# Optimization experiments

Measured on AMD Instinct MI355X. Metric: run time of the kernel, lower is better.

## Reference

```python
import jax, jax.numpy as jnp
import numpy as np

N = 16384
IN_DIM = 64
OUT_DIM = 64
BN_EPS = 1e-5
LEAKY_SLOPE = 0.01


def setup_inputs() -> dict:
    key = jax.random.key(0)
    k_g, k_h, k_w, k_b = jax.random.split(key, 4)
    g = jax.random.uniform(k_g, (N, N), dtype=jnp.float32)  # dense nonneg adjacency
    h = jax.random.normal(k_h, (N, IN_DIM), dtype=jnp.float32)
    W = jax.random.normal(k_w, (OUT_DIM, IN_DIM), dtype=jnp.float32) * (1.0 / np.sqrt(IN_DIM))
    b = jax.random.normal(k_b, (OUT_DIM,), dtype=jnp.float32) * 0.01
    gamma = jnp.ones((IN_DIM,), dtype=jnp.float32)
    beta = jnp.zeros((IN_DIM,), dtype=jnp.float32)
    return {"g": g, "h": h, "W": W, "b": b, "gamma": gamma, "beta": beta}


def reference(g, h, W, b, gamma, beta):
    # BatchNorm1d in training mode: batch statistics over the node axis
    mean = h.mean(axis=0)
    var = jnp.mean(jnp.square(h - mean), axis=0)  # biased variance, as torch BN
    hn = (h - mean) * (gamma / jnp.sqrt(var + BN_EPS)) + beta

    # g <- g + I  (add self-loops on the diagonal, no dense eye materialized)
    idx = jnp.arange(g.shape[0])
    ga = g.at[idx, idx].add(1.0)

    # D^{-1/2} A D^{-1/2}: torch builds diag matrices and does two N^3 matmuls;
    # mathematically identical row/column scaling (same values, O(N^2)).
    d_inv_sqrt = jax.lax.rsqrt(ga.sum(axis=1))  # [N]
    gn = ga * d_inv_sqrt[:, None] * d_inv_sqrt[None, :]

    # Linear projection, propagate, LeakyReLU
    hp = hn @ W.T + b                     # [N, out_dim]
    out = gn @ hp                         # [N, out_dim]
    return jnp.where(out >= 0, out, LEAKY_SLOPE * out)
```

## Files before the change

### kernel.cpp

```cpp
#include <hip/hip_runtime.h>
#include <hip/hip_bf16.h>

#define GN 16384
#define GDIM 64

typedef __attribute__((ext_vector_type(8))) short bf16x8;
typedef __attribute__((ext_vector_type(4))) float f32x4;

typedef __attribute__((address_space(1))) const void GASV;
typedef __attribute__((address_space(3))) void LASV;

__device__ __forceinline__ unsigned short f2bf(float x) {
    unsigned int u = __builtin_bit_cast(unsigned int, x);
    u += 0x7fffu + ((u >> 16) & 1u);
    return (unsigned short)(u >> 16);
}

__device__ __forceinline__ short f2bf_hw(float x) {
    __hip_bfloat16 b = __float2bfloat16(x);
    return (short)__builtin_bit_cast(unsigned short, b);
}

__global__ void bn_partial(const float* __restrict__ h, float* __restrict__ ps,
                           float* __restrict__ pq) {
    int b = blockIdx.x, t = threadIdx.x;
    int col = t & 63, wr = t >> 6;
    float s = 0.f, q = 0.f;
    int base = b * 64;
    for (int rep = 0; rep < 16; ++rep) {
        int row = base + wr + rep * 4;
        float v = h[row * GDIM + col];
        s += v; q += v * v;
    }
    __shared__ float ls[4][64], lq[4][64];
    ls[wr][col] = s; lq[wr][col] = q;
    __syncthreads();
    if (t < 64) {
        ps[b * 64 + t] = ls[0][t] + ls[1][t] + ls[2][t] + ls[3][t];
        pq[b * 64 + t] = lq[0][t] + lq[1][t] + lq[2][t] + lq[3][t];
    }
}

__global__ void bn_finalize(const float* __restrict__ ps, const float* __restrict__ pq,
                            const float* __restrict__ W, const float* __restrict__ bvec,
                            const float* __restrict__ gamma, const float* __restrict__ beta,
                            float* __restrict__ Wp, float* __restrict__ bp) {
    int t = threadIdx.x;
    __shared__ float s_s[64], s_t2[64];
    if (t < 64) {
        float S = 0.f, Q = 0.f;
        for (int b = 0; b < 256; ++b) { S += ps[b * 64 + t]; Q += pq[b * 64 + t]; }
        float mean = S * (1.0f / 16384.0f);
        float var  = Q * (1.0f / 16384.0f) - mean * mean;
        float sc   = gamma[t] * rsqrtf(var + 1e-5f);
        s_s[t]  = sc;
        s_t2[t] = beta[t] - mean * sc;
    }
    __syncthreads();
    for (int k = 0; k < 16; ++k) {
        int idx = t + k * 256;
        Wp[idx] = s_s[idx & 63] * W[idx];
    }
    if (t < 64) {
        float acc = bvec[t];
        for (int c = 0; c < 64; ++c) acc += s_t2[c] * W[t * 64 + c];
        bp[t] = acc;
    }
}

__global__ void linear_hp(const float* __restrict__ h, const float* __restrict__ Wp,
                          const float* __restrict__ bpr, float* __restrict__ hp) {
    __shared__ float lw[64][65];
    __shared__ float lh[16][65];
    int t = threadIdx.x;
    int rb = blockIdx.x * 16;
    for (int k = 0; k < 16; ++k) {
        int idx = t + k * 256;
        lw[idx >> 6][idx & 63] = Wp[idx];
    }
    for (int k = 0; k < 4; ++k) {
        int idx = t + k * 256;
        lh[idx >> 6][idx & 63] = h[rb * GDIM + idx];
    }
    __syncthreads();
    int o = t & 63, rg = t >> 6;
    float a0 = 0.f, a1 = 0.f, a2 = 0.f, a3 = 0.f;
    for (int c = 0; c < 64; ++c) {
        float wv = lw[o][c];
        a0 += lh[rg][c]      * wv;
        a1 += lh[rg + 4][c]  * wv;
        a2 += lh[rg + 8][c]  * wv;
        a3 += lh[rg + 12][c] * wv;
    }
    float bb = bpr[o];
    hp[(rb + rg) * GDIM + o]      = a0 + bb;
    hp[(rb + rg + 4) * GDIM + o]  = a1 + bb;
    hp[(rb + rg + 8) * GDIM + o]  = a2 + bb;
    hp[(rb + rg + 12) * GDIM + o] = a3 + bb;
}

__global__ void rowsum_dinv(const float* __restrict__ g, float* __restrict__ dinv) {
    int row = blockIdx.x, t = threadIdx.x;
    const f32x4* grow = (const f32x4*)(g + (size_t)row * GN);
    float s = 0.f;
    for (int k = 0; k < 16; ++k) {
        f32x4 v = grow[t + k * 256];
        s += (v[0] + v[1]) + (v[2] + v[3]);
    }
    for (int off = 32; off; off >>= 1) s += __shfl_down(s, off, 64);
    __shared__ float wsum[4];
    if ((t & 63) == 0) wsum[t >> 6] = s;
    __syncthreads();
    if (t == 0) {
        float tot = (wsum[0] + wsum[1]) + (wsum[2] + wsum[3]) + 1.0f;
        dinv[row] = rsqrtf(tot);
    }
}

__global__ void make_hsT(const float* __restrict__ hp, const float* __restrict__ dinv,
                         unsigned short* __restrict__ hsT) {
    __shared__ float tile[64][65];
    int t = threadIdx.x;
    int jb = blockIdx.x * 64;
    int o = t & 63, jg = t >> 6;
    for (int k = 0; k < 16; ++k) {
        int j = jg + k * 4;
        tile[j][o] = hp[(jb + j) * GDIM + o] * dinv[jb + j];
    }
    __syncthreads();
    int oo = t >> 2, q = t & 3;
    for (int k = 0; k < 16; ++k) {
        int j = q * 16 + k;
        hsT[(size_t)oo * GN + jb + j] = f2bf(tile[j][oo]);
    }
}

__global__ void __launch_bounds__(1024, 4) spmm_part(
    const float* __restrict__ g, const unsigned short* __restrict__ hsT,
    float* __restrict__ part)
{
    __shared__ unsigned short bs[2][64][520];

    int t = threadIdx.x;
    int lane = t & 63;
    int w = t >> 6;
    int itile = blockIdx.x >> 2;
    int split = blockIdx.x & 3;
    int rb = itile * 256;
    int kb = split * 4096;
    int l15 = lane & 15;
    int kg = lane >> 4;

    f32x4 acc[4];
    #pragma unroll
    for (int n = 0; n < 4; ++n)
        #pragma unroll
        for (int r = 0; r < 4; ++r) acc[n][r] = 0.f;

    const float* abase = g + (size_t)(rb + w * 16 + l15) * GN + kb + kg * 8;

    auto stage = [&](int kc, int buf) {
        int ck = kb + kc * 512;
        #pragma unroll
        for (int q = 0; q < 4; ++q) {
            int o = w * 4 + q;
            const char* src = (const char*)(hsT + (size_t)o * GN + ck) + lane * 16;
            __builtin_amdgcn_global_load_lds((GASV*)src, (LASV*)&bs[buf][o][0], 16, 0, 0);
        }
    };

    int c0 = itile & 7;
    stage(c0, 0);
    __syncthreads();

    for (int c = 0; c < 8; ++c) {
        int buf = c & 1;
        if (c < 7) stage((c + 1 + itile) & 7, buf ^ 1);

        int cbase = ((c + itile) & 7) * 512;
        for (int it = 0; it < 16; ++it) {
            int ko = it * 32 + kg * 8;
            bf16x8 bfr[4];
            #pragma unroll
            for (int n = 0; n < 4; ++n)
                bfr[n] = *(const bf16x8*)&bs[buf][n * 16 + l15][ko];
            const float* ap = abase + cbase + it * 32;
            f32x4 x0 = *(const f32x4*)ap;
            f32x4 x1 = *((const f32x4*)ap + 1);
            bf16x8 afr;
            afr[0] = f2bf_hw(x0[0]); afr[1] = f2bf_hw(x0[1]);
            afr[2] = f2bf_hw(x0[2]); afr[3] = f2bf_hw(x0[3]);
            afr[4] = f2bf_hw(x1[0]); afr[5] = f2bf_hw(x1[1]);
            afr[6] = f2bf_hw(x1[2]); afr[7] = f2bf_hw(x1[3]);
            #pragma unroll
            for (int n = 0; n < 4; ++n)
                acc[n] = __builtin_amdgcn_mfma_f32_16x16x32_bf16(afr, bfr[n], acc[n], 0, 0, 0);
        }
        __syncthreads();
    }

    float* pdst = part + (size_t)split * (GN * GDIM);
    #pragma unroll
    for (int n = 0; n < 4; ++n)
        #pragma unroll
        for (int r = 0; r < 4; ++r) {
            int i = rb + w * 16 + kg * 4 + r;
            int col = n * 16 + l15;
            pdst[(size_t)i * GDIM + col] = acc[n][r];
        }
}

__global__ void epilogue(const float* __restrict__ part, const float* __restrict__ hp,
                         const float* __restrict__ dinv, float* __restrict__ out) {
    int q = blockIdx.x * 256 + threadIdx.x;
    int i = q >> 4;
    int o = (q & 15) * 4;
    size_t off = (size_t)i * GDIM + o;
    const size_t S = (size_t)GN * GDIM;
    f32x4 s0 = *(const f32x4*)(part + off);
    f32x4 s1 = *(const f32x4*)(part + S + off);
    f32x4 s2 = *(const f32x4*)(part + 2 * S + off);
    f32x4 s3 = *(const f32x4*)(part + 3 * S + off);
    f32x4 hpv = *(const f32x4*)(hp + off);
    float di = dinv[i];
    f32x4 v = (s0 + s1) + (s2 + s3);
    #pragma unroll
    for (int r = 0; r < 4; ++r) {
        float x = di * (v[r] + di * hpv[r]);
        v[r] = (x >= 0.f) ? x : 0.01f * x;
    }
    *(f32x4*)(out + off) = v;
}

extern "C" void kernel_launch(void* const* d_in, const int* in_sizes, int n_in,
                              void* d_out, int out_size, void* d_ws, size_t ws_size,
                              hipStream_t stream) {
    const float* g     = (const float*)d_in[0];
    const float* h     = (const float*)d_in[1];
    const float* W     = (const float*)d_in[2];
    const float* b     = (const float*)d_in[3];
    const float* gamma = (const float*)d_in[4];
    const float* beta  = (const float*)d_in[5];
    float* out = (float*)d_out;

    float* ws   = (float*)d_ws;
    float* ps   = ws;
    float* pq   = ws + 16384;
    float* Wp   = ws + 32768;
    float* bp   = ws + 36864;
    float* dinv = ws + 36928;
    float* hp   = ws + 53312;
    unsigned short* hsT = (unsigned short*)(ws + 1101888);
    float* part = ws + 1626176;

    bn_partial  <<<256,   256, 0, stream>>>(h, ps, pq);
    bn_finalize <<<1,     256, 0, stream>>>(ps, pq, W, b, gamma, beta, Wp, bp);
    linear_hp   <<<1024,  256, 0, stream>>>(h, Wp, bp, hp);
    rowsum_dinv <<<16384, 256, 0, stream>>>(g, dinv);
    make_hsT    <<<256,   256, 0, stream>>>(hp, dinv, hsT);
    spmm_part   <<<256,  1024, 0, stream>>>(g, hsT, part);
    epilogue    <<<1024,  256, 0, stream>>>(part, hp, dinv, out);
}
```

Before: 400.2 us.

## Fuse linear and transpose, widen spmm row tiles, store bf16 partials

Merges the linear projection with the dinv-scaled bf16 transpose into one kernel, removing a launch and an hp round trip. The spmm kernel now gives each wave two 16-row A tiles (512 rows per block) and uses an 8-way K split, so each staged B chunk in LDS feeds twice as many MFMAs. Partial sums are written as bf16 across 8 splits instead of fp32 across 4, keeping partial traffic about the same. Storing partials in bf16 adds rounding error to the accumulated sums, and the doubled accumulators raise register pressure under the 1024-thread launch bound.

New measurement: 411.3 us. 2.8% more time.

```diff
diff --git a/kernel.cpp b/kernel.cpp
--- a/kernel.cpp
+++ b/kernel.cpp
@@ -6,6 +6,7 @@
 
 typedef __attribute__((ext_vector_type(8))) short bf16x8;
 typedef __attribute__((ext_vector_type(4))) float f32x4;
+typedef __attribute__((ext_vector_type(4))) unsigned short u16x4;
 
 typedef __attribute__((address_space(1))) const void GASV;
 typedef __attribute__((address_space(3))) void LASV;
@@ -19,6 +20,11 @@
 __device__ __forceinline__ short f2bf_hw(float x) {
     __hip_bfloat16 b = __float2bfloat16(x);
     return (short)__builtin_bit_cast(unsigned short, b);
+}
+
+__device__ __forceinline__ float bf2f(unsigned short u) {
+    unsigned int v = (unsigned int)u << 16;
+    return __builtin_bit_cast(float, v);
 }
 
 __global__ void bn_partial(const float* __restrict__ h, float* __restrict__ ps,
@@ -68,10 +74,30 @@
     }
 }
 
-__global__ void linear_hp(const float* __restrict__ h, const float* __restrict__ Wp,
-                          const float* __restrict__ bpr, float* __restrict__ hp) {
+__global__ void rowsum_dinv(const float* __restrict__ g, float* __restrict__ dinv) {
+    int row = blockIdx.x, t = threadIdx.x;
+    const f32x4* grow = (const f32x4*)(g + (size_t)row * GN);
+    float s = 0.f;
+    for (int k = 0; k < 16; ++k) {
+        f32x4 v = grow[t + k * 256];
+        s += (v[0] + v[1]) + (v[2] + v[3]);
+    }
+    for (int off = 32; off; off >>= 1) s += __shfl_down(s, off, 64);
+    __shared__ float wsum[4];
+    if ((t & 63) == 0) wsum[t >> 6] = s;
+    __syncthreads();
+    if (t == 0) {
+        float tot = (wsum[0] + wsum[1]) + (wsum[2] + wsum[3]) + 1.0f;
+        dinv[row] = rsqrtf(tot);
+    }
+}
+
+__global__ void linear_hsT(const float* __restrict__ h, const float* __restrict__ Wp,
+                           const float* __restrict__ bpr, const float* __restrict__ dinv,
+                           float* __restrict__ hp, unsigned short* __restrict__ hsT) {
     __shared__ float lw[64][65];
     __shared__ float lh[16][65];
+    __shared__ unsigned short ts[64][20];
     int t = threadIdx.x;
     int rb = blockIdx.x * 16;
     for (int k = 0; k < 16; ++k) {
@@ -93,71 +119,48 @@
         a3 += lh[rg + 12][c] * wv;
     }
     float bb = bpr[o];
-    hp[(rb + rg) * GDIM + o]      = a0 + bb;
-    hp[(rb + rg + 4) * GDIM + o]  = a1 + bb;
-    hp[(rb + rg + 8) * GDIM + o]  = a2 + bb;
-    hp[(rb + rg + 12) * GDIM + o] = a3 + bb;
-}
-
-__global__ void rowsum_dinv(const float* __restrict__ g, float* __restrict__ dinv) {
-    int row = blockIdx.x, t = threadIdx.x;
-    const f32x4* grow = (const f32x4*)(g + (size_t)row * GN);
-    float s = 0.f;
-    for (int k = 0; k < 16; ++k) {
-        f32x4 v = grow[t + k * 256];
-        s += (v[0] + v[1]) + (v[2] + v[3]);
-    }
-    for (int off = 32; off; off >>= 1) s += __shfl_down(s, off, 64);
-    __shared__ float wsum[4];
-    if ((t & 63) == 0) wsum[t >> 6] = s;
-    __syncthreads();
-    if (t == 0) {
-        float tot = (wsum[0] + wsum[1]) + (wsum[2] + wsum[3]) + 1.0f;
-        dinv[row] = rsqrtf(tot);
-    }
-}
-
-__global__ void make_hsT(const float* __restrict__ hp, const float* __restrict__ dinv,
-                         unsigned short* __restrict__ hsT) {
-    __shared__ float tile[64][65];
-    int t = threadIdx.x;
-    int jb = blockIdx.x * 64;
-    int o = t & 63, jg = t >> 6;
-    for (int k = 0; k < 16; ++k) {
-        int j = jg + k * 4;
-        tile[j][o] = hp[(jb + j) * GDIM + o] * dinv[jb + j];
-    }
-    __syncthreads();
-    int oo = t >> 2, q = t & 3;
-    for (int k = 0; k < 16; ++k) {
-        int j = q * 16 + k;
-        hsT[(size_t)oo * GN + jb + j] = f2bf(tile[j][oo]);
-    }
+    a0 += bb; a1 += bb; a2 += bb; a3 += bb;
+    hp[(rb + rg) * GDIM + o]      = a0;
+    hp[(rb + rg + 4) * GDIM + o]  = a1;
+    hp[(rb + rg + 8) * GDIM + o]  = a2;
+    hp[(rb + rg + 12) * GDIM + o] = a3;
+    ts[o][rg]      = f2bf(dinv[rb + rg]      * a0);
+    ts[o][rg + 4]  = f2bf(dinv[rb + rg + 4]  * a1);
+    ts[o][rg + 8]  = f2bf(dinv[rb + rg + 8]  * a2);
+    ts[o][rg + 12] = f2bf(dinv[rb + rg + 12] * a3);
+    __syncthreads();
+    int oo = t >> 2, j0 = (t & 3) * 4;
+    u16x4 v;
+    v[0] = ts[oo][j0]; v[1] = ts[oo][j0 + 1];
+    v[2] = ts[oo][j0 + 2]; v[3] = ts[oo][j0 + 3];
+    *(u16x4*)(hsT + (size_t)oo * GN + rb + j0) = v;
 }
 
 __global__ void __launch_bounds__(1024, 4) spmm_part(
     const float* __restrict__ g, const unsigned short* __restrict__ hsT,
-    float* __restrict__ part)
+    unsigned short* __restrict__ part)
 {
     __shared__ unsigned short bs[2][64][520];
 
     int t = threadIdx.x;
     int lane = t & 63;
     int w = t >> 6;
-    int itile = blockIdx.x >> 2;
-    int split = blockIdx.x & 3;
-    int rb = itile * 256;
-    int kb = split * 4096;
+    int itile = blockIdx.x >> 3;
+    int split = blockIdx.x & 7;
+    int rb = itile * 512;
+    int kb = split * 2048;
     int l15 = lane & 15;
     int kg = lane >> 4;
 
-    f32x4 acc[4];
-    #pragma unroll
-    for (int n = 0; n < 4; ++n)
-        #pragma unroll
-        for (int r = 0; r < 4; ++r) acc[n][r] = 0.f;
-
-    const float* abase = g + (size_t)(rb + w * 16 + l15) * GN + kb + kg * 8;
+    f32x4 acc[2][4];
+    #pragma unroll
+    for (int m = 0; m < 2; ++m)
+        #pragma unroll
+        for (int n = 0; n < 4; ++n)
+            #pragma unroll
+            for (int r = 0; r < 4; ++r) acc[m][n][r] = 0.f;
+
+    const float* abase = g + (size_t)(rb + w * 32 + l15) * GN + kb + kg * 8;
 
     auto stage = [&](int kc, int buf) {
         int ck = kb + kc * 512;
@@ -169,64 +172,73 @@
         }
     };
 
-    int c0 = itile & 7;
-    stage(c0, 0);
-    __syncthreads();
-
-    for (int c = 0; c < 8; ++c) {
+    stage(itile & 3, 0);
+    __syncthreads();
+
+    for (int c = 0; c < 4; ++c) {
         int buf = c & 1;
-        if (c < 7) stage((c + 1 + itile) & 7, buf ^ 1);
-
-        int cbase = ((c + itile) & 7) * 512;
+        if (c < 3) stage((c + 1 + itile) & 3, buf ^ 1);
+
+        int cbase = ((c + itile) & 3) * 512;
         for (int it = 0; it < 16; ++it) {
             int ko = it * 32 + kg * 8;
             bf16x8 bfr[4];
             #pragma unroll
             for (int n = 0; n < 4; ++n)
                 bfr[n] = *(const bf16x8*)&bs[buf][n * 16 + l15][ko];
-            const float* ap = abase + cbase + it * 32;
-            f32x4 x0 = *(const f32x4*)ap;
-            f32x4 x1 = *((const f32x4*)ap + 1);
-            bf16x8 afr;
-            afr[0] = f2bf_hw(x0[0]); afr[1] = f2bf_hw(x0[1]);
-            afr[2] = f2bf_hw(x0[2]); afr[3] = f2bf_hw(x0[3]);
-            afr[4] = f2bf_hw(x1[0]); afr[5] = f2bf_hw(x1[1]);
-            afr[6] = f2bf_hw(x1[2]); afr[7] = f2bf_hw(x1[3]);
-            #pragma unroll
-            for (int n = 0; n < 4; ++n)
-                acc[n] = __builtin_amdgcn_mfma_f32_16x16x32_bf16(afr, bfr[n], acc[n], 0, 0, 0);
+            #pragma unroll
+            for (int m = 0; m < 2; ++m) {
+                const float* ap = abase + (size_t)m * 16 * GN + cbase + it * 32;
+                f32x4 x0 = *(const f32x4*)ap;
+                f32x4 x1 = *((const f32x4*)ap + 1);
+                bf16x8 afr;
+                afr[0] = f2bf_hw(x0[0]); afr[1] = f2bf_hw(x0[1]);
+                afr[2] = f2bf_hw(x0[2]); afr[3] = f2bf_hw(x0[3]);
+                afr[4] = f2bf_hw(x1[0]); afr[5] = f2bf_hw(x1[1]);
+                afr[6] = f2bf_hw(x1[2]); afr[7] = f2bf_hw(x1[3]);
+                #pragma unroll
+                for (int n = 0; n < 4; ++n)
+                    acc[m][n] = __builtin_amdgcn_mfma_f32_16x16x32_bf16(afr, bfr[n], acc[m][n], 0, 0, 0);
+            }
         }
         __syncthreads();
     }
 
-    float* pdst = part + (size_t)split * (GN * GDIM);
-    #pragma unroll
-    for (int n = 0; n < 4; ++n)
-        #pragma unroll
-        for (int r = 0; r < 4; ++r) {
-            int i = rb + w * 16 + kg * 4 + r;
-            int col = n * 16 + l15;
-            pdst[(size_t)i * GDIM + col] = acc[n][r];
-        }
-}
-
-__global__ void epilogue(const float* __restrict__ part, const float* __restrict__ hp,
+    unsigned short* pdst = part + (size_t)split * (GN * GDIM);
+    #pragma unroll
+    for (int m = 0; m < 2; ++m)
+        #pragma unroll
+        for (int n = 0; n < 4; ++n)
+            #pragma unroll
+            for (int r = 0; r < 4; ++r) {
+                int i = rb + w * 32 + m * 16 + kg * 4 + r;
+                int col = n * 16 + l15;
+                pdst[(size_t)i * GDIM + col] = (unsigned short)f2bf_hw(acc[m][n][r]);
+            }
+}
+
+__global__ void epilogue(const unsigned short* __restrict__ part,
+                         const float* __restrict__ hp,
                          const float* __restrict__ dinv, float* __restrict__ out) {
     int q = blockIdx.x * 256 + threadIdx.x;
     int i = q >> 4;
     int o = (q & 15) * 4;
     size_t off = (size_t)i * GDIM + o;
     const size_t S = (size_t)GN * GDIM;
-    f32x4 s0 = *(const f32x4*)(part + off);
-    f32x4 s1 = *(const f32x4*)(part + S + off);
-    f32x4 s2 = *(const f32x4*)(part + 2 * S + off);
-    f32x4 s3 = *(const f32x4*)(part + 3 * S + off);
+    float s[4] = {0.f, 0.f, 0.f, 0.f};
+    #pragma unroll
+    for (int p0 = 0; p0 < 8; p0 += 2) {
+        u16x4 ua = *(const u16x4*)(part + p0 * S + off);
+        u16x4 ub = *(const u16x4*)(part + (p0 + 1) * S + off);
+        #pragma unroll
+        for (int r = 0; r < 4; ++r) s[r] += bf2f(ua[r]) + bf2f(ub[r]);
+    }
     f32x4 hpv = *(const f32x4*)(hp + off);
     float di = dinv[i];
-    f32x4 v = (s0 + s1) + (s2 + s3);
+    f32x4 v;
     #pragma unroll
     for (int r = 0; r < 4; ++r) {
-        float x = di * (v[r] + di * hpv[r]);
+        float x = di * (s[r] + di * hpv[r]);
         v[r] = (x >= 0.f) ? x : 0.01f * x;
     }
     *(f32x4*)(out + off) = v;
@@ -250,14 +262,13 @@
     float* bp   = ws + 36864;
     float* dinv = ws + 36928;
     float* hp   = ws + 53312;
-    unsigned short* hsT = (unsigned short*)(ws + 1101888);
-    float* part = ws + 1626176;
+    unsigned short* hsT  = (unsigned short*)(ws + 1101888);
+    unsigned short* part = (unsigned short*)(ws + 1363968);
 
     bn_partial  <<<256,   256, 0, stream>>>(h, ps, pq);
     bn_finalize <<<1,     256, 0, stream>>>(ps, pq, W, b, gamma, beta, Wp, bp);
-    linear_hp   <<<1024,  256, 0, stream>>>(h, Wp, bp, hp);
     rowsum_dinv <<<16384, 256, 0, stream>>>(g, dinv);
-    make_hsT    <<<256,   256, 0, stream>>>(hp, dinv, hsT);
+    linear_hsT  <<<1024,  256, 0, stream>>>(h, Wp, bp, dinv, hp, hsT);
     spmm_part   <<<256,  1024, 0, stream>>>(g, hsT, part);
     epilogue    <<<1024,  256, 0, stream>>>(part, hp, dinv, out);
 }
```
